# Optimization experiments

Measured on AMD Instinct MI355X. Metric: run time of the kernel, lower is better.

Reference implementation:

```python
import jax, jax.numpy as jnp
import numpy as np

EPS = 1e-3  # denominator regularizer for weighted mean/cov
DIST_SCALE = 10.0  # raw_call applies 10.0 * distsq before exp weighting

V, K, C, F = 100000, 40, 3, 32


def setup_inputs() -> dict:
    key = jax.random.key(0)
    k1, k2, k3, k4 = jax.random.split(key, 4)
    coordinates = jax.random.normal(k1, (V, C), dtype=jnp.float32)
    distsq = jax.random.uniform(k2, (V, K), dtype=jnp.float32)  # squared distances >= 0
    features = jax.random.uniform(k3, (V, F), dtype=jnp.float32)  # non-negative activations
    n_idxs = jax.random.randint(k4, (V, K), 0, V, dtype=jnp.int32)
    return {"coordinates": coordinates, "distsq": distsq, "features": features, "n_idxs": n_idxs}


def reference(coordinates, distsq, features, n_idxs):
    nV, nC = coordinates.shape
    nF = features.shape[1]
    # SelectWithDefault semantics: index -1 -> default 0
    valid = (n_idxs >= 0)
    idx = jnp.where(valid, n_idxs, 0)
    n_coords = jnp.where(valid[..., None], coordinates[idx], 0.0)  # V x K x C
    w = jnp.exp(-DIST_SCALE * distsq)  # V x K distance weights
    n_feat = jnp.where(valid[..., None], features[idx], 0.0) * w[..., None]  # V x K x F (feature weights)
    wsum = jnp.sum(n_feat, axis=1)  # V x F
    denom = wsum[:, :, None] + EPS  # V x F x 1
    # weighted first moment -> means, weighted second moment -> covariance
    means = jnp.einsum('vkf,vkc->vfc', n_feat, n_coords) / denom  # V x F x C
    second = jnp.einsum('vkf,vkc,vkd->vfcd', n_feat, n_coords, n_coords) / denom[..., None]  # V x F x C x C
    cov = second - means[:, :, :, None] * means[:, :, None, :]  # centered covariance
    out = jnp.concatenate([cov.reshape(nV, nF * nC * nC), means.reshape(nV, nF * nC)], axis=-1)
    return out
```

## Files before the change

### kernel.cpp

```cpp
#include <hip/hip_runtime.h>


constexpr int K = 40;
constexpr int C = 3;
constexpr int F = 32;
constexpr float EPS = 1e-3f;
constexpr float DIST_SCALE = 10.0f;
constexpr int OUT_PER_V = F * C * C + F * C;
constexpr int VPB = 8;
constexpr int PAIRS = VPB * K;

__global__ __launch_bounds__(256) void neighcov_kernel(
    const float* __restrict__ coords,
    const float* __restrict__ distsq,
    const float* __restrict__ features,
    const int*   __restrict__ nidx,
    float* __restrict__ out,
    int V)
{
    __shared__ float4 s_wxyz[PAIRS];
    __shared__ int    s_joff[PAIRS];

    const int tid   = threadIdx.x;
    const int vbase = blockIdx.x * VPB;
    const long long total_pairs = (long long)V * K;

    #pragma unroll
    for (int p = tid; p < PAIRS; p += 256) {
        const long long gp = (long long)vbase * K + p;
        int idx = -1;
        float d = 0.f;
        if (gp < total_pairs) {
            idx = nidx[gp];
            d   = distsq[gp];
        }
        const bool valid = (idx >= 0);
        const int j = valid ? idx : 0;
        const float w = valid ? __expf(-DIST_SCALE * d) : 0.f;
        const float x = coords[(size_t)j * 3 + 0];
        const float y = coords[(size_t)j * 3 + 1];
        const float z = coords[(size_t)j * 3 + 2];
        s_wxyz[p] = make_float4(w, x, y, z);
        s_joff[p] = j * F;
    }
    __syncthreads();

    const int f    = tid & (F - 1);
    const int vloc = tid >> 5;
    const int v    = vbase + vloc;
    if (v >= V) return;

    const float4* wp = &s_wxyz[vloc * K];
    const int*    jp = &s_joff[vloc * K];

    float wsum = 0.f;
    float m0 = 0.f, m1 = 0.f, m2 = 0.f;
    float s00 = 0.f, s01 = 0.f, s02 = 0.f, s11 = 0.f, s12 = 0.f, s22 = 0.f;

    #pragma unroll 8
    for (int k = 0; k < K; ++k) {
        const float4 q = wp[k];
        const int jo   = jp[k];
        const float feat = features[jo + f];
        const float fw = q.x * feat;
        const float x = q.y, y = q.z, z = q.w;
        const float fx = fw * x, fy = fw * y, fz = fw * z;
        wsum += fw;
        m0 += fx;        m1 += fy;        m2 += fz;
        s00 += fx * x;   s01 += fx * y;   s02 += fx * z;
        s11 += fy * y;   s12 += fy * z;   s22 += fz * z;
    }

    const float inv = 1.f / (wsum + EPS);
    const float mu0 = m0 * inv, mu1 = m1 * inv, mu2 = m2 * inv;
    const float c00 = s00 * inv - mu0 * mu0;
    const float c01 = s01 * inv - mu0 * mu1;
    const float c02 = s02 * inv - mu0 * mu2;
    const float c11 = s11 * inv - mu1 * mu1;
    const float c12 = s12 * inv - mu1 * mu2;
    const float c22 = s22 * inv - mu2 * mu2;

    float* o = out + (size_t)v * OUT_PER_V + f * 9;
    o[0] = c00; o[1] = c01; o[2] = c02;
    o[3] = c01; o[4] = c11; o[5] = c12;
    o[6] = c02; o[7] = c12; o[8] = c22;

    float* om = out + (size_t)v * OUT_PER_V + F * 9 + f * 3;
    om[0] = mu0; om[1] = mu1; om[2] = mu2;
}

extern "C" void kernel_launch(void* const* d_in, const int* in_sizes, int n_in,
                              void* d_out, int out_size, void* d_ws, size_t ws_size,
                              hipStream_t stream) {
    const float* coords   = (const float*)d_in[0];
    const float* distsq   = (const float*)d_in[1];
    const float* features = (const float*)d_in[2];
    const int*   nidx     = (const int*)d_in[3];
    float* out = (float*)d_out;

    const int V = in_sizes[0] / C;
    const int blocks = (V + VPB - 1) / VPB;

    neighcov_kernel<<<blocks, 256, 0, stream>>>(coords, distsq, features, nidx, out, V);
}
```

Baseline: 254.6 us.

## Assign four features per thread with float4 gathers and 32 vertices per block

Each thread now handles four consecutive features of one vertex and loads them with a single float4 gather, so each block covers 32 vertices instead of 8. The shared-memory staging uses a padded row stride (K+1) so that threads of different vertices avoid bank conflicts. The aim is fewer, wider global gather instructions and better amortisation of the index and coordinate staging. The cost is roughly four times the accumulator registers per thread, which may lower occupancy, and output stores that are more strided across lanes.

```diff
diff --git a/kernel.cpp b/kernel.cpp
--- a/kernel.cpp
+++ b/kernel.cpp
@@ -2,12 +2,13 @@
 
 
 constexpr int K = 40;
+constexpr int KP = K + 1;
 constexpr int C = 3;
 constexpr int F = 32;
 constexpr float EPS = 1e-3f;
 constexpr float DIST_SCALE = 10.0f;
 constexpr int OUT_PER_V = F * C * C + F * C;
-constexpr int VPB = 8;
+constexpr int VPB = 32;
 constexpr int PAIRS = VPB * K;
 
 __global__ __launch_bounds__(256) void neighcov_kernel(
@@ -18,8 +19,8 @@
     float* __restrict__ out,
     int V)
 {
-    __shared__ float4 s_wxyz[PAIRS];
-    __shared__ int    s_joff[PAIRS];
+    __shared__ float4 s_wxyz[VPB * KP];
+    __shared__ int    s_joff[VPB * KP];
 
     const int tid   = threadIdx.x;
     const int vbase = blockIdx.x * VPB;
@@ -27,7 +28,9 @@
 
     #pragma unroll
     for (int p = tid; p < PAIRS; p += 256) {
-        const long long gp = (long long)vbase * K + p;
+        const int vloc = p / K;
+        const int k    = p - vloc * K;
+        const long long gp = (long long)(vbase + vloc) * K + k;
         int idx = -1;
         float d = 0.f;
         if (gp < total_pairs) {
@@ -40,53 +43,63 @@
         const float x = coords[(size_t)j * 3 + 0];
         const float y = coords[(size_t)j * 3 + 1];
         const float z = coords[(size_t)j * 3 + 2];
-        s_wxyz[p] = make_float4(w, x, y, z);
-        s_joff[p] = j * F;
+        s_wxyz[vloc * KP + k] = make_float4(w, x, y, z);
+        s_joff[vloc * KP + k] = j * F;
     }
     __syncthreads();
 
-    const int f    = tid & (F - 1);
-    const int vloc = tid >> 5;
+    const int g    = tid & 7;
+    const int vloc = tid >> 3;
     const int v    = vbase + vloc;
     if (v >= V) return;
 
-    const float4* wp = &s_wxyz[vloc * K];
-    const int*    jp = &s_joff[vloc * K];
+    const float4* wp = &s_wxyz[vloc * KP];
+    const int*    jp = &s_joff[vloc * KP];
 
-    float wsum = 0.f;
-    float m0 = 0.f, m1 = 0.f, m2 = 0.f;
-    float s00 = 0.f, s01 = 0.f, s02 = 0.f, s11 = 0.f, s12 = 0.f, s22 = 0.f;
+    float wsum[4] = {0.f, 0.f, 0.f, 0.f};
+    float m0[4] = {0.f}, m1[4] = {0.f}, m2[4] = {0.f};
+    float s00[4] = {0.f}, s01[4] = {0.f}, s02[4] = {0.f};
+    float s11[4] = {0.f}, s12[4] = {0.f}, s22[4] = {0.f};
 
-    #pragma unroll 8
+    #pragma unroll 4
     for (int k = 0; k < K; ++k) {
         const float4 q = wp[k];
         const int jo   = jp[k];
-        const float feat = features[jo + f];
-        const float fw = q.x * feat;
+        const float4 ft = *(const float4*)(features + jo + 4 * g);
+        const float fv[4] = {ft.x, ft.y, ft.z, ft.w};
         const float x = q.y, y = q.z, z = q.w;
-        const float fx = fw * x, fy = fw * y, fz = fw * z;
-        wsum += fw;
-        m0 += fx;        m1 += fy;        m2 += fz;
-        s00 += fx * x;   s01 += fx * y;   s02 += fx * z;
-        s11 += fy * y;   s12 += fy * z;   s22 += fz * z;
+        #pragma unroll
+        for (int i = 0; i < 4; ++i) {
+            const float fw = fv[i] * q.x;
+            const float fx = fw * x, fy = fw * y, fz = fw * z;
+            wsum[i] += fw;
+            m0[i] += fx;       m1[i] += fy;       m2[i] += fz;
+            s00[i] += fx * x;  s01[i] += fx * y;  s02[i] += fx * z;
+            s11[i] += fy * y;  s12[i] += fy * z;  s22[i] += fz * z;
+        }
     }
 
-    const float inv = 1.f / (wsum + EPS);
-    const float mu0 = m0 * inv, mu1 = m1 * inv, mu2 = m2 * inv;
-    const float c00 = s00 * inv - mu0 * mu0;
-    const float c01 = s01 * inv - mu0 * mu1;
-    const float c02 = s02 * inv - mu0 * mu2;
-    const float c11 = s11 * inv - mu1 * mu1;
-    const float c12 = s12 * inv - mu1 * mu2;
-    const float c22 = s22 * inv - mu2 * mu2;
+    float* ov = out + (size_t)v * OUT_PER_V;
+    #pragma unroll
+    for (int i = 0; i < 4; ++i) {
+        const float inv = 1.f / (wsum[i] + EPS);
+        const float mu0 = m0[i] * inv, mu1 = m1[i] * inv, mu2 = m2[i] * inv;
+        const float c00 = s00[i] * inv - mu0 * mu0;
+        const float c01 = s01[i] * inv - mu0 * mu1;
+        const float c02 = s02[i] * inv - mu0 * mu2;
+        const float c11 = s11[i] * inv - mu1 * mu1;
+        const float c12 = s12[i] * inv - mu1 * mu2;
+        const float c22 = s22[i] * inv - mu2 * mu2;
 
-    float* o = out + (size_t)v * OUT_PER_V + f * 9;
-    o[0] = c00; o[1] = c01; o[2] = c02;
-    o[3] = c01; o[4] = c11; o[5] = c12;
-    o[6] = c02; o[7] = c12; o[8] = c22;
+        const int fglob = g * 4 + i;
+        float* o = ov + fglob * 9;
+        o[0] = c00; o[1] = c01; o[2] = c02;
+        o[3] = c01; o[4] = c11; o[5] = c12;
+        o[6] = c02; o[7] = c12; o[8] = c22;
 
-    float* om = out + (size_t)v * OUT_PER_V + F * 9 + f * 3;
-    om[0] = mu0; om[1] = mu1; om[2] = mu2;
+        float* om = ov + F * 9 + fglob * 3;
+        om[0] = mu0; om[1] = mu1; om[2] = mu2;
+    }
 }
 
 extern "C" void kernel_launch(void* const* d_in, const int* in_sizes, int n_in,
```

New measurement: 293.3 us. 15.2% more time.

## Stage gathered neighbor features in shared memory as fp16 via float4 loads

Applied to the files above, without the earlier changes.

Adds a cooperative gather phase in which each block loads the 32-float feature rows of all its neighbors with float4 loads, converts them to half precision and stores them in shared memory. The accumulation loop then reads features from shared memory instead of issuing scattered scalar global loads. The aim is wider, better-coalesced gathers and more memory-level parallelism, at the cost of an extra barrier, about 20KB more shared memory per block (which may limit occupancy), and fp16 rounding of the feature values.

```diff
diff --git a/kernel.cpp b/kernel.cpp
--- a/kernel.cpp
+++ b/kernel.cpp
@@ -1,4 +1,5 @@
 #include <hip/hip_runtime.h>
+#include <hip/hip_fp16.h>
 
 
 constexpr int K = 40;
@@ -8,7 +9,7 @@
 constexpr float DIST_SCALE = 10.0f;
 constexpr int OUT_PER_V = F * C * C + F * C;
 constexpr int VPB = 8;
-constexpr int PAIRS = VPB * K;
+constexpr int ROWS = VPB * K;
 
 __global__ __launch_bounds__(256) void neighcov_kernel(
     const float* __restrict__ coords,
@@ -18,19 +19,22 @@
     float* __restrict__ out,
     int V)
 {
-    __shared__ float4 s_wxyz[PAIRS];
-    __shared__ int    s_joff[PAIRS];
+    __shared__ float4 s_wxyz[ROWS];
+    __shared__ int    s_joff[ROWS];
+    __shared__ __half s_feat[ROWS * F];
 
     const int tid   = threadIdx.x;
     const int vbase = blockIdx.x * VPB;
-    const long long total_pairs = (long long)V * K;
 
     #pragma unroll
-    for (int p = tid; p < PAIRS; p += 256) {
-        const long long gp = (long long)vbase * K + p;
+    for (int p = tid; p < ROWS; p += 256) {
+        const int vloc = p / K;
+        const int k    = p - vloc * K;
+        const int vg   = vbase + vloc;
         int idx = -1;
         float d = 0.f;
-        if (gp < total_pairs) {
+        if (vg < V) {
+            const size_t gp = (size_t)vg * K + k;
             idx = nidx[gp];
             d   = distsq[gp];
         }
@@ -45,13 +49,26 @@
     }
     __syncthreads();
 
+    #pragma unroll
+    for (int q = tid; q < ROWS * 8; q += 256) {
+        const int r    = q >> 3;
+        const int quad = q & 7;
+        const int jo   = s_joff[r];
+        const float4 ft = *(const float4*)(features + jo + 4 * quad);
+        union { __half2 h2[2]; uint2 u; } pk;
+        pk.h2[0] = __floats2half2_rn(ft.x, ft.y);
+        pk.h2[1] = __floats2half2_rn(ft.z, ft.w);
+        *(uint2*)&s_feat[r * F + 4 * quad] = pk.u;
+    }
+    __syncthreads();
+
     const int f    = tid & (F - 1);
     const int vloc = tid >> 5;
     const int v    = vbase + vloc;
     if (v >= V) return;
 
     const float4* wp = &s_wxyz[vloc * K];
-    const int*    jp = &s_joff[vloc * K];
+    const __half* fp = &s_feat[vloc * K * F + f];
 
     float wsum = 0.f;
     float m0 = 0.f, m1 = 0.f, m2 = 0.f;
@@ -60,8 +77,7 @@
     #pragma unroll 8
     for (int k = 0; k < K; ++k) {
         const float4 q = wp[k];
-        const int jo   = jp[k];
-        const float feat = features[jo + f];
+        const float feat = __half2float(fp[k * F]);
         const float fw = q.x * feat;
         const float x = q.y, y = q.z, z = q.w;
         const float fx = fw * x, fy = fw * y, fz = fw * z;
```

New measurement: 279.3 us. 9.7% more time.
